# Optimization experiments

Measured on AMD Instinct MI355X. Metric: run time of the kernel, lower is better.

## Reference

```python
import jax, jax.numpy as jnp
import numpy as np

B, S, HID = 2, 4096, 1024
NH, HD = 16, 64
R = 2  # dilation_rate


def setup_inputs() -> dict:
    key = jax.random.key(0)
    ks = jax.random.split(key, 6)
    sc = 0.02
    return {
        "hidden_states": jax.random.normal(ks[0], (B, S, HID), jnp.float32),
        "Wq": jax.random.normal(ks[1], (HID, HID), jnp.float32) * sc,
        "Wk": jax.random.normal(ks[2], (HID, HID), jnp.float32) * sc,
        "Wv": jax.random.normal(ks[3], (HID, HID), jnp.float32) * sc,
        "Wo": jax.random.normal(ks[4], (HID, HID), jnp.float32) * sc,
        "bo": jnp.zeros((HID,), jnp.float32),
    }


def reference(hidden_states, Wq, Wk, Wv, Wo, bo):
    bsz, q_len, _ = hidden_states.shape
    # projections (torch Linear: y = x @ W.T)
    q = jnp.einsum('bsh,oh->bso', hidden_states, Wq).reshape(bsz, q_len, NH, HD).transpose(0, 2, 1, 3)
    k = jnp.einsum('bsh,oh->bso', hidden_states, Wk).reshape(bsz, q_len, NH, HD).transpose(0, 2, 1, 3)
    v = jnp.einsum('bsh,oh->bso', hidden_states, Wv).reshape(bsz, q_len, NH, HD).transpose(0, 2, 1, 3)
    # strided dilation gather (indices 0, R, 2R, ...)
    q = q[:, :, ::R, :]
    k = k[:, :, ::R, :]
    v = v[:, :, ::R, :]
    sd = q.shape[2]  # dilated length
    # SDPA with is_causal=True over the dilated subsequence
    scores = jnp.einsum('bhqd,bhkd->bhqk', q, k) / np.sqrt(HD).astype(np.float32)
    causal = jnp.tril(jnp.ones((sd, sd), bool))
    scores = jnp.where(causal, scores, jnp.finfo(scores.dtype).min)
    probs = jax.nn.softmax(scores, axis=-1)
    attn = jnp.einsum('bhqk,bhkd->bhqd', probs, v)  # [B, H, sd, HD]
    attn = attn.transpose(0, 2, 1, 3).reshape(bsz, sd, HID)
    # scatter back into zero-initialized full-length tensor
    full = jnp.zeros((bsz, q_len, HID), attn.dtype).at[:, ::R, :].set(attn)
    return jnp.einsum('bsh,oh->bso', full, Wo) + bo
```

## Files before the change

### kernel.cpp

```cpp
#include <hip/hip_runtime.h>
#include <cstdint>

typedef unsigned short u16;
typedef unsigned int u32;
typedef __attribute__((ext_vector_type(8))) short short8;
typedef __attribute__((ext_vector_type(4))) float f32x4;
typedef __attribute__((ext_vector_type(4))) unsigned short u16x4;
typedef __attribute__((ext_vector_type(4))) u32 u32x4;
typedef __attribute__((ext_vector_type(2))) u32 u32x2;

#define S_ 4096
#define SD 2048

__device__ __forceinline__ u16 f2bf(float f) {
  union { float f; u32 u; } v; v.f = f;
  u32 r = v.u + 0x7fffu + ((v.u >> 16) & 1u);
  return (u16)(r >> 16);
}
__device__ __forceinline__ float bf2f(u16 x) {
  union { u32 u; float f; } v; v.u = ((u32)x) << 16; return v.f;
}
#if __has_builtin(__builtin_amdgcn_cvt_pk_bf16_f32)
__device__ __forceinline__ u32 pkbf(float a, float b) {
  auto r = __builtin_amdgcn_cvt_pk_bf16_f32(a, b);
  u32 o; __builtin_memcpy(&o, &r, 4); return o;
}
#else
__device__ __forceinline__ u32 pkbf(float a, float b) {
  union { float f; u32 u; } ua, ub; ua.f = a; ub.f = b;
  return __builtin_amdgcn_perm(ub.u + 0x8000u, ua.u + 0x8000u, 0x07060302u);
}
#endif
__device__ __forceinline__ f32x4 mfma16(short8 a, short8 b, f32x4 c) {
  return __builtin_amdgcn_mfma_f32_16x16x32_bf16(a, b, c, 0, 0, 0);
}
__device__ __forceinline__ void async16(const void* g, void* l) {
  __builtin_amdgcn_global_load_lds((__attribute__((address_space(1))) void*)g,
                                   (__attribute__((address_space(3))) void*)l,
                                   16, 0, 0);
}

__global__ __launch_bounds__(256) void cast_all(const float* __restrict__ hs,
                                                const float* __restrict__ Wq,
                                                const float* __restrict__ Wk,
                                                const float* __restrict__ Wv,
                                                const float* __restrict__ Wo,
                                                u16* __restrict__ dstW,
                                                u16* __restrict__ dstX) {
  int bid = blockIdx.x;
  if (bid < 4096) {
    int gid = bid * 256 + threadIdx.x;
    int wsel = gid >> 18;
    int off  = (gid & 262143) * 4;
    const float* src = (wsel == 0) ? Wq : (wsel == 1) ? Wk : (wsel == 2) ? Wv : Wo;
    float scl = (wsel == 0) ? 0.18033688f : 1.0f;
    f32x4 v = *(const f32x4*)(src + off);
    u16x4 o; o.x = f2bf(v.x * scl); o.y = f2bf(v.y * scl);
    o.z = f2bf(v.z * scl); o.w = f2bf(v.w * scl);
    *(u16x4*)(dstW + (size_t)wsel * 1048576 + off) = o;
  } else {
    int gid = (bid - 4096) * 256 + threadIdx.x;
    int e = gid * 4;
    int m = e >> 10, col = e & 1023;
    int b = m >> 11, sm = m & 2047;
    const float* src = hs + ((size_t)(b * S_ + 2 * sm) << 10) + col;
    f32x4 v = *(const f32x4*)src;
    u16x4 o; o.x = f2bf(v.x); o.y = f2bf(v.y); o.z = f2bf(v.z); o.w = f2bf(v.w);
    *(u16x4*)(dstX + ((size_t)m << 10) + col) = o;
  }
}

__device__ __forceinline__ void gemm_body128(const u16* __restrict__ A,
                                             const u16* __restrict__ B,
                                             u16* __restrict__ C, int N,
                                             int bm, int bn, char* lA, char* lB) {
  const int tid = threadIdx.x, lane = tid & 63, w = tid >> 6;
  const int quad = lane >> 4, l15 = lane & 15;
  const int wm = (w & 1) * 64, wn = (w >> 1) * 64;
  f32x4 acc[4][4] = {};

  auto stage = [&](int buf, int k0) {
#pragma unroll
    for (int i = 0; i < 2; i++) {
      int p = i * 256 + tid;
      int row = p >> 2, cp = p & 3;
      int c = cp ^ ((row ^ (row >> 2)) & 3);
      async16(A + (size_t)(bm + row) * 1024 + k0 + c * 8,
              lA + buf * 8192 + i * 4096 + w * 1024);
      async16(B + (size_t)(bn + row) * 1024 + k0 + c * 8,
              lB + buf * 8192 + i * 4096 + w * 1024);
    }
  };

  stage(0, 0);
#pragma unroll 1
  for (int kt = 0; kt < 32; kt++) {
    __syncthreads();
    if (kt + 1 < 32) stage((kt + 1) & 1, (kt + 1) * 32);
    const char* A_ = lA + (kt & 1) * 8192;
    const char* B_ = lB + (kt & 1) * 8192;
    short8 af[4], bf[4];
#pragma unroll
    for (int mi = 0; mi < 4; mi++) {
      int row = wm + mi * 16 + l15;
      af[mi] = *(const short8*)(A_ + (row * 4 + (quad ^ ((row ^ (row >> 2)) & 3))) * 16);
    }
#pragma unroll
    for (int ni = 0; ni < 4; ni++) {
      int row = wn + ni * 16 + l15;
      bf[ni] = *(const short8*)(B_ + (row * 4 + (quad ^ ((row ^ (row >> 2)) & 3))) * 16);
    }
#pragma unroll
    for (int mi = 0; mi < 4; mi++)
#pragma unroll
      for (int ni = 0; ni < 4; ni++)
        acc[mi][ni] = mfma16(af[mi], bf[ni], acc[mi][ni]);
  }
#pragma unroll
  for (int mi = 0; mi < 4; mi++)
#pragma unroll
    for (int ni = 0; ni < 4; ni++) {
      int m0 = bm + wm + mi * 16 + quad * 4;
      int n = bn + wn + ni * 16 + l15;
#pragma unroll
      for (int r = 0; r < 4; r++)
        C[(size_t)(m0 + r) * N + n] = f2bf(acc[mi][ni][r]);
    }
}

__global__ __launch_bounds__(256) void qkv_gemm(const u16* __restrict__ X,
                                                const u16* __restrict__ Wbf,
                                                u16* __restrict__ QK,
                                                u16* __restrict__ Vt) {
  __shared__ __align__(16) char lA[16384];
  __shared__ __align__(16) char lB[16384];
  int bid = blockIdx.x;
  if (bid < 512) {
    gemm_body128(X, Wbf, QK, 2048, (bid >> 4) * 128, (bid & 15) * 128, lA, lB);
  } else {
    int b2 = bid - 512;
    gemm_body128(Wbf + 2 * 1048576, X, Vt, 4096, (b2 >> 5) * 128, (b2 & 31) * 128, lA, lB);
  }
}

__global__ __launch_bounds__(256) void oproj(const u16* __restrict__ A,
                                             const u16* __restrict__ B,
                                             const float* __restrict__ bo,
                                             float* __restrict__ out) {
  __shared__ __align__(16) char lA[8192];
  __shared__ __align__(16) char lB[16384];
  const int tid = threadIdx.x, lane = tid & 63, w = tid >> 6;
  const int quad = lane >> 4, l15 = lane & 15;
  const int bm = blockIdx.y * 64, bn = blockIdx.x * 128;
  const int wm = (w & 1) * 32, wn = (w >> 1) * 64;
  f32x4 acc[2][4] = {};

  auto stage = [&](int buf, int k0) {
    {
      int row = tid >> 2, cp = tid & 3;
      int c = cp ^ ((row ^ (row >> 2)) & 3);
      async16(A + (size_t)(bm + row) * 1024 + k0 + c * 8, lA + buf * 4096 + w * 1024);
    }
#pragma unroll
    for (int i = 0; i < 2; i++) {
      int p = i * 256 + tid;
      int row = p >> 2, cp = p & 3;
      int c = cp ^ ((row ^ (row >> 2)) & 3);
      async16(B + (size_t)(bn + row) * 1024 + k0 + c * 8, lB + buf * 8192 + i * 4096 + w * 1024);
    }
  };

  stage(0, 0);
#pragma unroll 1
  for (int kt = 0; kt < 32; kt++) {
    __syncthreads();
    if (kt + 1 < 32) stage((kt + 1) & 1, (kt + 1) * 32);
    const char* A_ = lA + (kt & 1) * 4096;
    const char* B_ = lB + (kt & 1) * 8192;
    short8 af[2], bf[4];
#pragma unroll
    for (int mi = 0; mi < 2; mi++) {
      int row = wm + mi * 16 + l15;
      af[mi] = *(const short8*)(A_ + (row * 4 + (quad ^ ((row ^ (row >> 2)) & 3))) * 16);
    }
#pragma unroll
    for (int ni = 0; ni < 4; ni++) {
      int row = wn + ni * 16 + l15;
      bf[ni] = *(const short8*)(B_ + (row * 4 + (quad ^ ((row ^ (row >> 2)) & 3))) * 16);
    }
#pragma unroll
    for (int mi = 0; mi < 2; mi++)
#pragma unroll
      for (int ni = 0; ni < 4; ni++)
        acc[mi][ni] = mfma16(af[mi], bf[ni], acc[mi][ni]);
  }
#pragma unroll
  for (int mi = 0; mi < 2; mi++)
#pragma unroll
    for (int ni = 0; ni < 4; ni++) {
      int n = bn + wn + ni * 16 + l15;
      float bias = bo[n];
#pragma unroll
      for (int r = 0; r < 4; r++) {
        int m = bm + wm + mi * 16 + quad * 4 + r;
        int bb = m >> 11, sm = m & 2047;
        size_t grow = ((size_t)(bb * S_ + 2 * sm)) << 10;
        out[grow + n] = acc[mi][ni][r] + bias;
        out[grow + 1024 + n] = bias;
      }
    }
}

__global__ __launch_bounds__(256) void attn8(const u16* __restrict__ QK,
                                             const u16* __restrict__ Vt,
                                             u16* __restrict__ O,
                                             float* __restrict__ Op0,
                                             u16* __restrict__ Op1,
                                             float* __restrict__ lp) {
  __shared__ __align__(16) char lK[2][8192];
  __shared__ __align__(16) char lV[2][8192];
  const int tid = threadIdx.x, lane = tid & 63, w = tid >> 6;
  const int quad = lane >> 4, l15 = lane & 15;
  const int h = blockIdx.x, b = blockIdx.y;
  const int z = (int)blockIdx.z;
  int qt, chunk, c0, c1;
  if (z < 32) {
    qt = 31 - (z >> 1); chunk = z & 1;
    if (chunk == 0) { c0 = 0; c1 = 15; } else { c0 = 16; c1 = qt; }
  } else {
    qt = 47 - z; chunk = 0; c0 = 0; c1 = qt;
  }
  const bool par = (z < 32);
  const int qb = qt * 64 + w * 16;

  const u16* qp = QK + (size_t)(b * SD + qb + l15) * 2048 + h * 64 + quad * 8;
  short8 qf0 = *(const short8*)qp;
  short8 qf1 = *(const short8*)(qp + 32);

  auto stageK = [&](int buf, int kb) {
#pragma unroll
    for (int i = 0; i < 2; i++) {
      int p = (w * 2 + i) * 64 + lane;
      int row = p >> 3, c = (p & 7) ^ (row & 7);
      async16(QK + (size_t)(b * SD + kb + row) * 2048 + 1024 + h * 64 + c * 8,
              lK[buf] + (w * 2 + i) * 1024);
    }
  };

  const int vd = tid >> 2, vg = tid & 3;
  const u16* vgbase = Vt + (size_t)(h * 64 + vd) * 4096 + b * SD;
  const int vs = vd & 7;
  const int cb0 = (vg & 1) * 2;
  const int cb1 = cb0 + 4;
  const int inn = (vg >> 1) * 8;
  const int aw0 = vd * 128 + ((cb0     ^ vs) * 16) + inn;
  const int aw1 = vd * 128 + (((cb0+1) ^ vs) * 16) + inn;
  const int aw2 = vd * 128 + ((cb1     ^ vs) * 16) + inn;
  const int aw3 = vd * 128 + (((cb1+1) ^ vs) * 16) + inn;

  u32x4 nv0, nv1;
  auto loadV = [&](int kb) {
    nv0 = *(const u32x4*)(vgbase + kb + vg * 8);
    nv1 = *(const u32x4*)(vgbase + kb + 32 + vg * 8);
  };
  auto writeV = [&](int buf) {
    char* Vn = lV[buf];
    *(u32x2*)(Vn + aw0) = u32x2{nv0.x, nv0.y};
    *(u32x2*)(Vn + aw1) = u32x2{nv0.z, nv0.w};
    *(u32x2*)(Vn + aw2) = u32x2{nv1.x, nv1.y};
    *(u32x2*)(Vn + aw3) = u32x2{nv1.z, nv1.w};
  };

  f32x4 oacc[4] = {};
  float l4[4] = {0.f, 0.f, 0.f, 0.f};

  stageK(0, c0 * 64);
  loadV(c0 * 64);
  writeV(0);

#pragma unroll 1
  for (int kt = c0; kt <= c1; kt++) {
    __syncthreads();
    if (kt + 1 <= c1) {
      stageK((kt + 1) & 1, (kt + 1) * 64);
      loadV((kt + 1) * 64);
    }
    const char* K_ = lK[kt & 1];
    const char* V_ = lV[kt & 1];

    f32x4 s[4];
#pragma unroll
    for (int m = 0; m < 4; m++) {
      int key = m * 16 + l15;
      short8 kf0 = *(const short8*)(K_ + (key * 8 + (quad ^ (key & 7))) * 16);
      short8 kf1 = *(const short8*)(K_ + (key * 8 + ((4 + quad) ^ (key & 7))) * 16);
      f32x4 a = {};
      a = mfma16(kf0, qf0, a);
      a = mfma16(kf1, qf1, a);
      s[m] = a;
    }
    if (kt == qt) {
      int qrel = w * 16 + l15;
#pragma unroll
      for (int m = 0; m < 4; m++)
#pragma unroll
        for (int r = 0; r < 4; r++)
          if (m * 16 + quad * 4 + r > qrel) s[m][r] = -1e30f;
    }
    float pr[4][4];
#pragma unroll
    for (int m = 0; m < 4; m++) {
#pragma unroll
      for (int r = 0; r < 4; r++) pr[m][r] = exp2f(s[m][r]);
      l4[m] += (pr[m][0] + pr[m][1]) + (pr[m][2] + pr[m][3]);
    }
    u32 pw[8];
#pragma unroll
    for (int m = 0; m < 4; m++) {
      pw[m * 2]     = pkbf(pr[m][0], pr[m][1]);
      pw[m * 2 + 1] = pkbf(pr[m][2], pr[m][3]);
    }
    short8 pf0, pf1;
    __builtin_memcpy(&pf0, &pw[0], 16);
    __builtin_memcpy(&pf1, &pw[4], 16);

#pragma unroll
    for (int m = 0; m < 4; m++) {
      int dr = m * 16 + l15;
      short8 vf0 = *(const short8*)(V_ + (dr * 128 + ((quad     ^ (dr & 7)) * 16)));
      short8 vf1 = *(const short8*)(V_ + (dr * 128 + (((4+quad) ^ (dr & 7)) * 16)));
      oacc[m] = mfma16(vf0, pf0, oacc[m]);
      oacc[m] = mfma16(vf1, pf1, oacc[m]);
    }
    if (kt + 1 <= c1) writeV((kt + 1) & 1);
  }

  float l = (l4[0] + l4[1]) + (l4[2] + l4[3]);
  l += __shfl_xor(l, 16, 64);
  l += __shfl_xor(l, 32, 64);

  if (!par) {
    float inv = 1.0f / l;
    u16* op = O + (size_t)(b * SD + qb + l15) * 1024 + h * 64;
#pragma unroll
    for (int m = 0; m < 4; m++) {
      u16x4 ov;
#pragma unroll
      for (int r = 0; r < 4; r++) ov[r] = f2bf(oacc[m][r] * inv);
      *(u16x4*)(op + m * 16 + quad * 4) = ov;
    }
  } else {
    int rq = b * 1024 + (qb - 1024 + l15);
    if (chunk == 0) {
      float* p0 = Op0 + ((size_t)rq << 10) + h * 64 + quad * 4;
#pragma unroll
      for (int m = 0; m < 4; m++)
        *(f32x4*)(p0 + m * 16) = oacc[m];
    } else {
      u16* p1 = Op1 + ((size_t)rq << 10) + h * 64 + quad * 4;
#pragma unroll
      for (int m = 0; m < 4; m++) {
        u16x4 ov;
#pragma unroll
        for (int r = 0; r < 4; r++) ov[r] = f2bf(oacc[m][r]);
        *(u16x4*)(p1 + m * 16) = ov;
      }
    }
    if (quad == 0) lp[chunk * 32768 + rq * 16 + h] = l;
  }
}

__global__ __launch_bounds__(256) void combine_po(const float* __restrict__ Op0,
                                                  const u16* __restrict__ Op1,
                                                  const float* __restrict__ lp,
                                                  u16* __restrict__ O) {
  int gid = blockIdx.x * 256 + threadIdx.x;
  int row = gid >> 8;
  int d0 = (gid & 255) * 4;
  int hh = d0 >> 6;
  float l = lp[row * 16 + hh] + lp[32768 + row * 16 + hh];
  float inv = 1.0f / l;
  f32x4 a = *(const f32x4*)(Op0 + ((size_t)row << 10) + d0);
  u16x4 b1 = *(const u16x4*)(Op1 + ((size_t)row << 10) + d0);
  int bb = row >> 10, qr = row & 1023;
  u16* op = O + ((size_t)(bb * SD + 1024 + qr) << 10) + d0;
  u16x4 o;
#pragma unroll
  for (int r = 0; r < 4; r++)
    o[r] = f2bf((a[r] + bf2f(b1[r])) * inv);
  *(u16x4*)op = o;
}

extern "C" void kernel_launch(void* const* d_in, const int* in_sizes, int n_in,
                              void* d_out, int out_size, void* d_ws, size_t ws_size,
                              hipStream_t stream) {
  (void)in_sizes; (void)n_in; (void)out_size; (void)ws_size;
  const float* hs = (const float*)d_in[0];
  const float* Wq = (const float*)d_in[1];
  const float* Wk = (const float*)d_in[2];
  const float* Wv = (const float*)d_in[3];
  const float* Wo = (const float*)d_in[4];
  const float* bo = (const float*)d_in[5];
  float* out = (float*)d_out;
  char* ws = (char*)d_ws;

  u16* Xbf = (u16*)ws;
  u16* Wbf = (u16*)(ws + (8u << 20));
  u16* QKb = (u16*)(ws + (16u << 20));
  u16* Vtb = (u16*)(ws + (32u << 20));
  u16* Ob  = (u16*)(ws + (40u << 20));

  float* Op0 = (float*)ws;
  float* lp  = (float*)(ws + (8u << 20));
  u16*   Op1 = (u16*)(ws + (9u << 20));

  cast_all<<<8192, 256, 0, stream>>>(hs, Wq, Wk, Wv, Wo, Wbf, Xbf);
  qkv_gemm<<<768, 256, 0, stream>>>(Xbf, Wbf, QKb, Vtb);
  attn8<<<dim3(16, 2, 48), 256, 0, stream>>>(QKb, Vtb, Ob, Op0, Op1, lp);
  combine_po<<<2048, 256, 0, stream>>>(Op0, Op1, lp, Ob);
  oproj<<<dim3(8, 64), 256, 0, stream>>>(Ob, Wbf + 3 * 1048576, bo, out);
}
```

Measured before the change: 197.3 us.

## Double attention query tile to 128 rows per block with split-K rebalance

The attention kernel now has each wave process 32 query rows (two 16-row MFMA tiles) instead of 16, so each staged K/V tile in LDS is reused for twice as many queries. The grid shrinks from 48 to 24 z-blocks, with the split of the long query tiles into two key chunks recomputed for 128-row tiles, and the causal mask now covers two diagonal key tiles. It adds a launch-bounds occupancy hint of 3 blocks. The cost is doubled accumulator registers and fewer blocks, which may reduce occupancy and load balance on a part with many CUs.

```diff
diff --git a/kernel.cpp b/kernel.cpp
--- a/kernel.cpp
+++ b/kernel.cpp
@@ -211,12 +211,12 @@
     }
 }
 
-__global__ __launch_bounds__(256) void attn8(const u16* __restrict__ QK,
-                                             const u16* __restrict__ Vt,
-                                             u16* __restrict__ O,
-                                             float* __restrict__ Op0,
-                                             u16* __restrict__ Op1,
-                                             float* __restrict__ lp) {
+__global__ __launch_bounds__(256, 3) void attn9(const u16* __restrict__ QK,
+                                                const u16* __restrict__ Vt,
+                                                u16* __restrict__ O,
+                                                float* __restrict__ Op0,
+                                                u16* __restrict__ Op1,
+                                                float* __restrict__ lp) {
   __shared__ __align__(16) char lK[2][8192];
   __shared__ __align__(16) char lV[2][8192];
   const int tid = threadIdx.x, lane = tid & 63, w = tid >> 6;
@@ -224,18 +224,23 @@
   const int h = blockIdx.x, b = blockIdx.y;
   const int z = (int)blockIdx.z;
   int qt, chunk, c0, c1;
-  if (z < 32) {
-    qt = 31 - (z >> 1); chunk = z & 1;
-    if (chunk == 0) { c0 = 0; c1 = 15; } else { c0 = 16; c1 = qt; }
+  if (z < 16) {
+    qt = 15 - (z >> 1); chunk = z & 1;
+    if (chunk == 0) { c0 = 0; c1 = qt; } else { c0 = qt + 1; c1 = 2 * qt + 1; }
   } else {
-    qt = 47 - z; chunk = 0; c0 = 0; c1 = qt;
-  }
-  const bool par = (z < 32);
-  const int qb = qt * 64 + w * 16;
-
-  const u16* qp = QK + (size_t)(b * SD + qb + l15) * 2048 + h * 64 + quad * 8;
-  short8 qf0 = *(const short8*)qp;
-  short8 qf1 = *(const short8*)(qp + 32);
+    qt = 23 - z; chunk = 0; c0 = 0; c1 = 2 * qt + 1;
+  }
+  const bool par = (z < 16);
+  const int qb = qt * 128 + w * 32;
+  const int qt2 = 2 * qt;
+
+  short8 qf[2][2];
+#pragma unroll
+  for (int n = 0; n < 2; n++) {
+    const u16* qp = QK + (size_t)(b * SD + qb + n * 16 + l15) * 2048 + h * 64 + quad * 8;
+    qf[n][0] = *(const short8*)qp;
+    qf[n][1] = *(const short8*)(qp + 32);
+  }
 
   auto stageK = [&](int buf, int kb) {
 #pragma unroll
@@ -271,102 +276,107 @@
     *(u32x2*)(Vn + aw3) = u32x2{nv1.z, nv1.w};
   };
 
-  f32x4 oacc[4] = {};
-  float l4[4] = {0.f, 0.f, 0.f, 0.f};
+  f32x4 oacc[2][4] = {};
+  f32x4 l4v[2] = {};
+  const f32x4 zf = {};
 
   stageK(0, c0 * 64);
   loadV(c0 * 64);
   writeV(0);
+  const int J = c1 - c0;
 
 #pragma unroll 1
-  for (int kt = c0; kt <= c1; kt++) {
+  for (int j = 0; j <= J; j++) {
+    const int kt = c0 + j;
     __syncthreads();
-    if (kt + 1 <= c1) {
-      stageK((kt + 1) & 1, (kt + 1) * 64);
+    if (j + 1 <= J) {
+      stageK((j + 1) & 1, (kt + 1) * 64);
       loadV((kt + 1) * 64);
     }
-    const char* K_ = lK[kt & 1];
-    const char* V_ = lV[kt & 1];
-
-    f32x4 s[4];
+    const char* K_ = lK[j & 1];
+    const char* V_ = lV[j & 1];
+    const bool diag = (kt >= qt2);
+
+    u32 pw[2][8];
 #pragma unroll
     for (int m = 0; m < 4; m++) {
       int key = m * 16 + l15;
       short8 kf0 = *(const short8*)(K_ + (key * 8 + (quad ^ (key & 7))) * 16);
       short8 kf1 = *(const short8*)(K_ + (key * 8 + ((4 + quad) ^ (key & 7))) * 16);
-      f32x4 a = {};
-      a = mfma16(kf0, qf0, a);
-      a = mfma16(kf1, qf1, a);
-      s[m] = a;
-    }
-    if (kt == qt) {
-      int qrel = w * 16 + l15;
-#pragma unroll
-      for (int m = 0; m < 4; m++)
-#pragma unroll
-        for (int r = 0; r < 4; r++)
-          if (m * 16 + quad * 4 + r > qrel) s[m][r] = -1e30f;
-    }
-    float pr[4][4];
-#pragma unroll
-    for (int m = 0; m < 4; m++) {
-#pragma unroll
-      for (int r = 0; r < 4; r++) pr[m][r] = exp2f(s[m][r]);
-      l4[m] += (pr[m][0] + pr[m][1]) + (pr[m][2] + pr[m][3]);
-    }
-    u32 pw[8];
-#pragma unroll
-    for (int m = 0; m < 4; m++) {
-      pw[m * 2]     = pkbf(pr[m][0], pr[m][1]);
-      pw[m * 2 + 1] = pkbf(pr[m][2], pr[m][3]);
-    }
-    short8 pf0, pf1;
-    __builtin_memcpy(&pf0, &pw[0], 16);
-    __builtin_memcpy(&pf1, &pw[4], 16);
+#pragma unroll
+      for (int n = 0; n < 2; n++) {
+        f32x4 a = mfma16(kf0, qf[n][0], zf);
+        a = mfma16(kf1, qf[n][1], a);
+        if (diag) {
+          int qrel = w * 32 + n * 16 + l15;
+          int kd = (kt - qt2) * 64 + m * 16 + quad * 4;
+#pragma unroll
+          for (int r = 0; r < 4; r++)
+            if (kd + r > qrel) a[r] = -1e30f;
+        }
+        f32x4 p;
+#pragma unroll
+        for (int r = 0; r < 4; r++) p[r] = exp2f(a[r]);
+        l4v[n] += p;
+        pw[n][m * 2]     = pkbf(p[0], p[1]);
+        pw[n][m * 2 + 1] = pkbf(p[2], p[3]);
+      }
+    }
+    short8 pf[2][2];
+#pragma unroll
+    for (int n = 0; n < 2; n++) {
+      __builtin_memcpy(&pf[n][0], &pw[n][0], 16);
+      __builtin_memcpy(&pf[n][1], &pw[n][4], 16);
+    }
 
 #pragma unroll
     for (int m = 0; m < 4; m++) {
       int dr = m * 16 + l15;
       short8 vf0 = *(const short8*)(V_ + (dr * 128 + ((quad     ^ (dr & 7)) * 16)));
       short8 vf1 = *(const short8*)(V_ + (dr * 128 + (((4+quad) ^ (dr & 7)) * 16)));
-      oacc[m] = mfma16(vf0, pf0, oacc[m]);
-      oacc[m] = mfma16(vf1, pf1, oacc[m]);
-    }
-    if (kt + 1 <= c1) writeV((kt + 1) & 1);
-  }
-
-  float l = (l4[0] + l4[1]) + (l4[2] + l4[3]);
-  l += __shfl_xor(l, 16, 64);
-  l += __shfl_xor(l, 32, 64);
-
-  if (!par) {
-    float inv = 1.0f / l;
-    u16* op = O + (size_t)(b * SD + qb + l15) * 1024 + h * 64;
-#pragma unroll
-    for (int m = 0; m < 4; m++) {
-      u16x4 ov;
-#pragma unroll
-      for (int r = 0; r < 4; r++) ov[r] = f2bf(oacc[m][r] * inv);
-      *(u16x4*)(op + m * 16 + quad * 4) = ov;
-    }
-  } else {
-    int rq = b * 1024 + (qb - 1024 + l15);
-    if (chunk == 0) {
-      float* p0 = Op0 + ((size_t)rq << 10) + h * 64 + quad * 4;
-#pragma unroll
-      for (int m = 0; m < 4; m++)
-        *(f32x4*)(p0 + m * 16) = oacc[m];
-    } else {
-      u16* p1 = Op1 + ((size_t)rq << 10) + h * 64 + quad * 4;
+#pragma unroll
+      for (int n = 0; n < 2; n++) {
+        oacc[n][m] = mfma16(vf0, pf[n][0], oacc[n][m]);
+        oacc[n][m] = mfma16(vf1, pf[n][1], oacc[n][m]);
+      }
+    }
+    if (j + 1 <= J) writeV((j + 1) & 1);
+  }
+
+#pragma unroll
+  for (int n = 0; n < 2; n++) {
+    float l = (l4v[n][0] + l4v[n][1]) + (l4v[n][2] + l4v[n][3]);
+    l += __shfl_xor(l, 16, 64);
+    l += __shfl_xor(l, 32, 64);
+    if (!par) {
+      float inv = 1.0f / l;
+      u16* op = O + (size_t)(b * SD + qb + n * 16 + l15) * 1024 + h * 64;
 #pragma unroll
       for (int m = 0; m < 4; m++) {
         u16x4 ov;
 #pragma unroll
-        for (int r = 0; r < 4; r++) ov[r] = f2bf(oacc[m][r]);
-        *(u16x4*)(p1 + m * 16) = ov;
+        for (int r = 0; r < 4; r++) ov[r] = f2bf(oacc[n][m][r] * inv);
+        *(u16x4*)(op + m * 16 + quad * 4) = ov;
       }
-    }
-    if (quad == 0) lp[chunk * 32768 + rq * 16 + h] = l;
+    } else {
+      int rq = b * 1024 + (qb + n * 16 + l15 - 1024);
+      if (chunk == 0) {
+        float* p0 = Op0 + ((size_t)rq << 10) + h * 64 + quad * 4;
+#pragma unroll
+        for (int m = 0; m < 4; m++)
+          *(f32x4*)(p0 + m * 16) = oacc[n][m];
+      } else {
+        u16* p1 = Op1 + ((size_t)rq << 10) + h * 64 + quad * 4;
+#pragma unroll
+        for (int m = 0; m < 4; m++) {
+          u16x4 ov;
+#pragma unroll
+          for (int r = 0; r < 4; r++) ov[r] = f2bf(oacc[n][m][r]);
+          *(u16x4*)(p1 + m * 16) = ov;
+        }
+      }
+      if (quad == 0) lp[chunk * 32768 + rq * 16 + h] = l;
+    }
   }
 }
 
@@ -416,7 +426,7 @@
 
   cast_all<<<8192, 256, 0, stream>>>(hs, Wq, Wk, Wv, Wo, Wbf, Xbf);
   qkv_gemm<<<768, 256, 0, stream>>>(Xbf, Wbf, QKb, Vtb);
-  attn8<<<dim3(16, 2, 48), 256, 0, stream>>>(QKb, Vtb, Ob, Op0, Op1, lp);
+  attn9<<<dim3(16, 2, 24), 256, 0, stream>>>(QKb, Vtb, Ob, Op0, Op1, lp);
   combine_po<<<2048, 256, 0, stream>>>(Op0, Op1, lp, Ob);
   oproj<<<dim3(8, 64), 256, 0, stream>>>(Ob, Wbf + 3 * 1048576, bo, out);
 }
```

Result: no change. 200.9 us (+1.9%).
